# Kernel tuning notes

Hardware: AMD Instinct MI355X
Metric: run time of the kernel (lower is better)

The kernel has to match this reference:

```python
import jax, jax.numpy as jnp
import numpy as np

# ---- static physical configuration (matches init_kwargs param dict) ----
NX = NY = 513
NL = 3
N_ENS = 4
LX = LY = 5120.0e3
DX = LX / (NX - 1)
DY = LY / (NY - 1)
F0 = 9.375e-5
BETA = 1.754e-11
A2 = 0.0
A4 = 2.0e9
DELTA_EK = 2.0
TAU0 = 2.0e-5
BCCO = 0.2
ZFBC = BCCO / (1.0 + 0.5 * BCCO)
DT = 600.0
NUM_STEPS = 4
HEIGHTS = np.array([350.0, 750.0, 2900.0])
RED_G = np.array([0.025, 0.0125])

JAC_COEF = 1.0 / (F0 * DX * DY)
HYPERDIFF_COEF = A4 / F0**2 / DX**6
BOTTOM_FRICTION_COEF = DELTA_EK / (2.0 * abs(F0) * DX**2 * (-HEIGHTS[-1]))


def _build_constants():
    """Precompute stratification / mode / Helmholtz matrices (float64 numpy, cast to f32)."""
    A = np.zeros((NL, NL))
    A[0, 0] = 1.0 / (HEIGHTS[0] * RED_G[0])
    A[0, 1] = -1.0 / (HEIGHTS[0] * RED_G[0])
    for i in range(1, NL - 1):
        A[i, i - 1] = -1.0 / (HEIGHTS[i] * RED_G[i - 1])
        A[i, i] = 1.0 / HEIGHTS[i] * (1.0 / RED_G[i] + 1.0 / RED_G[i - 1])
        A[i, i + 1] = -1.0 / (HEIGHTS[i] * RED_G[i])
    A[-1, -1] = 1.0 / (HEIGHTS[NL - 1] * RED_G[NL - 2])
    A[-1, -2] = -1.0 / (HEIGHTS[NL - 1] * RED_G[NL - 2])
    lam_r, R = np.linalg.eig(A)
    lam_l, L = np.linalg.eig(A.T)
    lam_r, R, lam_l, L = lam_r.real, R.real, lam_l.real, L.real
    # align left eigenvectors with right eigenvalue ordering (biorthogonality)
    order = np.array([int(np.argmin(np.abs(lam_l - lr))) for lr in lam_r])
    L = L[:, order]
    Cl2m = np.diag(1.0 / np.diag(L.T @ R)) @ L.T
    Cm2l = R
    lambd = lam_r
    # DST-I eigenvalues of the 5-point Laplacian on the interior grid
    xg, yg = np.meshgrid(np.arange(1, NX - 1), np.arange(1, NY - 1), indexing='ij')
    lap_dst = (2 * (np.cos(np.pi / (NX - 1) * xg) - 1) / DX**2
               + 2 * (np.cos(np.pi / (NY - 1) * yg) - 1) / DY**2)
    helm_dst = lap_dst[None] / F0**2 - lambd[:, None, None]  # (nl, nx-2, ny-2)

    def np_dstI1D(x):
        N = x.shape[-1]
        xp = np.zeros(x.shape[:-1] + (N + 2,))
        xp[..., 1:-1] = x
        return np.fft.irfft(-1j * xp, n=2 * (N + 1), axis=-1, norm='ortho')[..., 1:N + 1]

    def np_dstI2D(x):
        return np.swapaxes(np_dstI1D(np.swapaxes(np_dstI1D(x), -1, -2)), -1, -2)

    const = np.ones((NL, NX, NY)) / (NX * NY)
    s = np.zeros_like(const)
    s[:, 1:-1, 1:-1] = np_dstI2D(np_dstI2D(const[:, 1:-1, 1:-1]) / helm_dst)
    hom_sol = (const + s * lambd[:, None, None])[:-1]  # (nl-1, nx, ny)
    M = (Cm2l[1:] - Cm2l[:-1])[:NL - 1, :NL - 1] * hom_sol.mean((1, 2))[None, :]
    alpha = -np.linalg.inv(M) @ (Cm2l[1:, :-1] - Cm2l[:-1, :-1])
    # wind forcing: curl(tau)/(f0*H1) on interior points; tau_y = 0, tau_x(y) only
    tau_x = -TAU0 * np.cos(2 * np.pi * (np.arange(NY) + 0.5) / NY)[None, :] * np.ones((NX, NY))
    dtaux_dy = (tau_x[1:-1, 2:] - tau_x[1:-1, :-2]) / (2 * DY)
    wind = (-dtaux_dy / (F0 * HEIGHTS[0]))[None]  # (1, nx-2, ny-2)
    f32 = lambda a: jnp.asarray(a, jnp.float32)
    return dict(A=f32(A), Cl2m=f32(Cl2m), Cm2l=f32(Cm2l), helmoltz_dst=f32(helm_dst),
                alpha_matrix=f32(alpha), homogeneous_sol=f32(hom_sol), wind_forcing=f32(wind))


# ---------------- stencil ops ----------------

def _pad11(x):
    return jnp.pad(x, [(0, 0)] * (x.ndim - 2) + [(1, 1), (1, 1)])


def laplacian_h_nobc(f):
    # unscaled 5-point Laplacian, interior values only: (..., nx-2, ny-2)
    return (f[..., 2:, 1:-1] + f[..., :-2, 1:-1] + f[..., 1:-1, 2:] + f[..., 1:-1, :-2]
            - 4.0 * f[..., 1:-1, 1:-1])


def laplacian_h(f, fc):
    # full-grid Laplacian with partial-slip boundary treatment (coefficient fc = zfbc)
    lap = _pad11(laplacian_h_nobc(f))
    lap = lap.at[..., 0, :].set(fc * (f[..., 1, :] - f[..., 0, :]))
    lap = lap.at[..., -1, :].set(fc * (f[..., -2, :] - f[..., -1, :]))
    lap = lap.at[..., :, 0].set(fc * (f[..., :, 1] - f[..., :, 0]))
    lap = lap.at[..., :, -1].set(fc * (f[..., :, -2] - f[..., :, -1]))
    return lap


def laplacian_h_boundaries(f, fc):
    # boundary Laplacian values, concat order: x=0 (y interior), x=-1, y=0 (full x), y=-1
    return jnp.concatenate([
        fc * (f[..., 1, 1:-1] - f[..., 0, 1:-1]),
        fc * (f[..., -2, 1:-1] - f[..., -1, 1:-1]),
        fc * (f[..., :, 1] - f[..., :, 0]),
        fc * (f[..., :, -2] - f[..., :, -1])], axis=-1)


def jacobi_h(f, g):
    # Arakawa 9-point Jacobian J(f, g), interior values (..., nx-2, ny-2)
    dx_f = f[..., 2:, :] - f[..., :-2, :]
    dx_g = g[..., 2:, :] - g[..., :-2, :]
    dy_f = f[..., 2:] - f[..., :-2]
    dy_g = g[..., 2:] - g[..., :-2]
    return ((dx_f[..., 1:-1] * dy_g[..., 1:-1, :] - dx_g[..., 1:-1] * dy_f[..., 1:-1, :])
            + (f[..., 2:, 1:-1] * dy_g[..., 2:, :] - f[..., :-2, 1:-1] * dy_g[..., :-2, :])
            - (f[..., 1:-1, 2:] * dx_g[..., 2:] - f[..., 1:-1, :-2] * dx_g[..., :-2])
            + (g[..., 1:-1, 2:] * dx_f[..., 2:] - g[..., 1:-1, :-2] * dx_f[..., :-2])
            - (g[..., 2:, 1:-1] * dy_f[..., 2:, :] - g[..., :-2, 1:-1] * dy_f[..., :-2, :])) / 12.0


# ---------------- DST-I elliptic solve ----------------

def dstI1D(x):
    N = x.shape[-1]
    z = jnp.zeros(x.shape[:-1] + (1,), x.dtype)
    xp = jnp.concatenate([z, x, z], axis=-1)
    return jnp.fft.irfft(-1j * xp.astype(jnp.complex64), n=2 * (N + 1), axis=-1,
                         norm='ortho')[..., 1:N + 1]


def dstI2D(x):
    return jnp.swapaxes(dstI1D(jnp.swapaxes(dstI1D(x), -1, -2)), -1, -2)


def inverse_elliptic_dst(f, op_dst):
    return dstI2D(dstI2D(f) / op_dst)


# ---------------- QG time derivative ----------------

def _time_derivatives(y, A, Cl2m, Cm2l, helm_dst, alpha, hom_sol, wind):
    q, p = y[0], y[1]  # (..., nl, nx, ny)
    # advection + hyperdiffusion RHS on interior (a_2 == 0 branch skipped as in source)
    rhs = JAC_COEF * jacobi_h(q, p)
    delta2_p = laplacian_h(p, ZFBC)
    rhs = rhs - HYPERDIFF_COEF * laplacian_h_nobc(laplacian_h(delta2_p, ZFBC))
    rhs = rhs.at[..., 0:1, :, :].add(wind)
    rhs = rhs.at[..., -1:, :, :].add(BOTTOM_FRICTION_COEF * laplacian_h_nobc(p[..., -1:, :, :]))
    dq = _pad11(rhs)
    # layers -> modes, DST Helmholtz inversion, homogeneous-solution correction
    rhs_h = jnp.einsum('ij,...jxy->...ixy', Cl2m, dq)
    dp_modes = _pad11(inverse_elliptic_dst(rhs_h[..., 1:-1, 1:-1], helm_dst))
    mean_m = dp_modes[..., :-1, :, :].mean((-2, -1))  # (..., nl-1)
    dalpha = jnp.einsum('ij,...j->...i', alpha, mean_m)[..., None, None]
    dp_modes = dp_modes.at[..., :-1, :, :].add(dalpha * hom_sol)
    dp = jnp.einsum('ij,...jxy->...ixy', Cm2l, dp_modes)
    # boundary vorticity update
    dp_bound = jnp.concatenate([dp[..., 0, 1:-1], dp[..., -1, 1:-1],
                                dp[..., :, 0], dp[..., :, -1]], axis=-1)
    delta_p_bound = laplacian_h_boundaries(dp / (F0 * DX)**2, ZFBC)
    dq_bound = delta_p_bound - jnp.einsum('ij,...jl->...il', A, dp_bound)
    ny2 = NY - 2
    dq = dq.at[..., 0, 1:-1].set(dq_bound[..., :ny2])
    dq = dq.at[..., -1, 1:-1].set(dq_bound[..., ny2:2 * ny2])
    dq = dq.at[..., :, 0].set(dq_bound[..., 2 * ny2:2 * ny2 + NX])
    dq = dq.at[..., :, -1].set(dq_bound[..., 2 * ny2 + NX:2 * ny2 + 2 * NX])
    return jnp.stack((dq, dp), 0)


def _forecast(y0, t, A, Cl2m, Cm2l, helm_dst, alpha, hom_sol, wind):
    deriv = lambda y: _time_derivatives(y, A, Cl2m, Cm2l, helm_dst, alpha, hom_sol, wind)

    def step(y, dt_):
        k1 = deriv(y)
        k2 = deriv(y + 0.5 * dt_ * k1)
        k3 = deriv(y + 0.5 * dt_ * k2)
        k4 = deriv(y + dt_ * k3)
        y_next = y + (dt_ / 6.0) * (k1 + 2.0 * k2 + 2.0 * k3 + k4)
        return y_next, y_next

    _, traj = jax.lax.scan(step, y0, t[1:] - t[:-1])
    return jnp.concatenate([y0[None], traj], axis=0)  # (T, 2, n_ens, nl, nx, ny)


def setup_inputs() -> dict:
    key = jax.random.key(0)
    y0 = 0.1 * jax.random.normal(key, (2, N_ENS, NL, NX, NY), dtype=jnp.float32)
    t = jnp.arange(NUM_STEPS + 1, dtype=jnp.float32) * DT
    consts = _build_constants()
    return dict(y0=y0, t=t, **consts)


def reference(y0, t, A, Cl2m, Cm2l, helmoltz_dst, alpha_matrix, homogeneous_sol, wind_forcing):
    return _forecast(y0, t, A, Cl2m, Cm2l, helmoltz_dst, alpha_matrix,
                     homogeneous_sol, wind_forcing)
```

## Files before the change

kernel.cpp:

```cpp
#include <hip/hip_runtime.h>
#include <math.h>

#define NXY 513
#define NIN 511
#define NL3 3
#define NE4 4
#define NB 12
#define GLD 512

static constexpr long FS  = (long)NE4 * NL3 * NXY * NXY;
static constexpr long GSZ = (long)NB * GLD * GLD;
static constexpr int  NSTEPS = 4;

static constexpr double dF0 = 9.375e-05;
static constexpr double dDX = 10000.0;
static constexpr float ZFBCf     = (float)(0.2 / (1.0 + 0.5 * 0.2));
static constexpr float JACCf     = (float)(1.0 / (dF0 * dDX * dDX));
static constexpr float HYPCf     = (float)(2.0e9 / (dF0 * dF0) / (dDX*dDX*dDX*dDX*dDX*dDX));
static constexpr float BFCf      = (float)(2.0 / (2.0 * dF0 * dDX * dDX * (-2900.0)));
static constexpr float INVF0DX2f = (float)(1.0 / ((dF0 * dDX) * (dF0 * dDX)));

typedef short  bf16x8 __attribute__((ext_vector_type(8)));
typedef float  f32x4  __attribute__((ext_vector_type(4)));
typedef unsigned int u32;
typedef __attribute__((address_space(1))) const u32 GAS;
typedef __attribute__((address_space(3))) u32 LAS;
#define GLDS(gp, lp) __builtin_amdgcn_global_load_lds((GAS*)(gp), (LAS*)(lp), 16, 0, 0)

__device__ __forceinline__ unsigned short f2bf(float x) {
    unsigned int u = __float_as_uint(x);
    return (unsigned short)((u + 0x7FFFu + ((u >> 16) & 1u)) >> 16);
}
__device__ __forceinline__ float bf2f(unsigned short h) {
    return __uint_as_float(((unsigned int)h) << 16);
}

__global__ void initS_kernel(unsigned short* __restrict__ Sh, unsigned short* __restrict__ Sl) {
    int k = blockIdx.x * 256 + threadIdx.x;
    int n = blockIdx.y;
    if (k >= GLD || n >= GLD) return;
    float v = 0.f;
    if (n < NIN && k < NIN) {
        int m = ((n + 1) * (k + 1)) & 1023;
        v = (float)(0.0625 * sin(M_PI * (double)m / 512.0));
    }
    unsigned short hs = f2bf(v);
    Sh[n * GLD + k] = hs;
    Sl[n * GLD + k] = f2bf(v - bf2f(hs));
}

__global__ __launch_bounds__(256) void fused_rhs(
    float* __restrict__ kq, const float* __restrict__ q, const float* __restrict__ p,
    const float* __restrict__ wind)
{
    __shared__ float ps[22][72];
    __shared__ float qs[22][72];
    __shared__ float l1[22][72];
    __shared__ float l2[22][72];
    const int c  = blockIdx.z;
    const int x0 = 1 + blockIdx.y * 16;
    const int y0 = 1 + blockIdx.x * 64;
    const int t  = threadIdx.x;
    const size_t off = (size_t)c * NXY * NXY;
    const float* pp = p + off;
    const float* qp = q + off;

    for (int idx = t; idx < 22 * 70; idx += 256) {
        int i = idx / 70, j = idx % 70;
        int gx = x0 - 3 + i, gy = y0 - 3 + j;
        bool in = (gx >= 0 && gx < NXY && gy >= 0 && gy < NXY);
        size_t go = (size_t)gx * NXY + gy;
        ps[i][j] = in ? pp[go] : 0.f;
        qs[i][j] = in ? qp[go] : 0.f;
    }
    __syncthreads();

#define LAPBC(a, i, j, gx, gy) \
    ((gy) == 0       ? ZFBCf * (a[i][(j)+1] - a[i][j]) : \
     (gy) == NXY-1   ? ZFBCf * (a[i][(j)-1] - a[i][j]) : \
     (gx) == 0       ? ZFBCf * (a[(i)+1][j] - a[i][j]) : \
     (gx) == NXY-1   ? ZFBCf * (a[(i)-1][j] - a[i][j]) : \
     a[(i)+1][j] + a[(i)-1][j] + a[i][(j)+1] + a[i][(j)-1] - 4.f * a[i][j])

    for (int idx = t; idx < 20 * 68; idx += 256) {
        int i = 1 + idx / 68, j = 1 + idx % 68;
        int gx = x0 - 3 + i, gy = y0 - 3 + j;
        float v = 0.f;
        if (gx >= 0 && gx < NXY && gy >= 0 && gy < NXY) v = LAPBC(ps, i, j, gx, gy);
        l1[i][j] = v;
    }
    __syncthreads();

    for (int idx = t; idx < 18 * 66; idx += 256) {
        int i = 2 + idx / 66, j = 2 + idx % 66;
        int gx = x0 - 3 + i, gy = y0 - 3 + j;
        float v = 0.f;
        if (gx >= 0 && gx < NXY && gy >= 0 && gy < NXY) v = LAPBC(l1, i, j, gx, gy);
        l2[i][j] = v;
    }
    __syncthreads();
#undef LAPBC

    const int l = c % NL3;
    for (int idx = t; idx < 16 * 64; idx += 256) {
        int i = 3 + idx / 64, j = 3 + idx % 64;
        int gx = x0 - 3 + i, gy = y0 - 3 + j;
        if (gx > NIN || gy > NIN) continue;
        float fmm=qs[i-1][j-1], fm0=qs[i-1][j], fmp=qs[i-1][j+1];
        float f0m=qs[i][j-1],                    f0p=qs[i][j+1];
        float fpm=qs[i+1][j-1], fp0=qs[i+1][j], fpp=qs[i+1][j+1];
        float gmm=ps[i-1][j-1], gm0=ps[i-1][j], gmp=ps[i-1][j+1];
        float g0m=ps[i][j-1],   g00=ps[i][j],   g0p=ps[i][j+1];
        float gpm=ps[i+1][j-1], gp0=ps[i+1][j], gpp=ps[i+1][j+1];
        float J1 = (fp0 - fm0) * (g0p - g0m) - (gp0 - gm0) * (f0p - f0m);
        float J2 = fp0 * (gpp - gpm) - fm0 * (gmp - gmm);
        float J3 = f0p * (gpp - gmp) - f0m * (gpm - gmm);
        float J4 = g0p * (fpp - fmp) - g0m * (fpm - fmm);
        float J5 = gp0 * (fpp - fpm) - gm0 * (fmp - fmm);
        float jac = (J1 + J2 - J3 + J4 - J5) * (1.0f / 12.0f);
        float lap3 = l2[i+1][j] + l2[i-1][j] + l2[i][j+1] + l2[i][j-1] - 4.f * l2[i][j];
        float v = JACCf * jac - HYPCf * lap3;
        if (l == 0)       v += wind[(size_t)(gx-1) * NIN + (gy-1)];
        if (l == NL3-1)   v += BFCf * (gp0 + gm0 + g0p + g0m - 4.f * g00);
        kq[off + (size_t)gx * NXY + gy] = v;
    }
}

__global__ void l2m_kernel(unsigned short* __restrict__ Gh, unsigned short* __restrict__ Gl,
                           const float* __restrict__ kq, const float* __restrict__ Cl2m) {
    int ry = blockIdx.x * blockDim.x + threadIdx.x;
    int rx = blockIdx.y * blockDim.y + threadIdx.y;
    int e = blockIdx.z;
    size_t go = (size_t)(e * NL3) * GLD * GLD + (size_t)rx * GLD + ry;
    if (rx >= NIN || ry >= NIN) {
        for (int i = 0; i < 3; ++i) { Gh[go + (size_t)i*GLD*GLD] = 0; Gl[go + (size_t)i*GLD*GLD] = 0; }
        return;
    }
    size_t base = ((size_t)(e * NL3) * NXY + (rx + 1)) * NXY + (ry + 1);
    float f0 = kq[base];
    float f1 = kq[base + (size_t)NXY*NXY];
    float f2 = kq[base + 2*(size_t)NXY*NXY];
    float v[3];
    v[0] = Cl2m[0]*f0 + Cl2m[1]*f1 + Cl2m[2]*f2;
    v[1] = Cl2m[3]*f0 + Cl2m[4]*f1 + Cl2m[5]*f2;
    v[2] = Cl2m[6]*f0 + Cl2m[7]*f1 + Cl2m[8]*f2;
#pragma unroll
    for (int i = 0; i < 3; ++i) {
        unsigned short hs = f2bf(v[i]);
        Gh[go + (size_t)i*GLD*GLD] = hs;
        Gl[go + (size_t)i*GLD*GLD] = f2bf(v[i] - bf2f(hs));
    }
}

#define EPLD 68
__global__ __launch_bounds__(256, 3) void gemm_dst(
    const unsigned short* __restrict__ Ah, const unsigned short* __restrict__ Al,
    const unsigned short* __restrict__ Sh, const unsigned short* __restrict__ Sl,
    unsigned short* __restrict__ Ch, unsigned short* __restrict__ Cl,
    float* __restrict__ Cf, const float* __restrict__ helm)
{
    __shared__ __attribute__((aligned(16))) char ldsraw[32768];
    float* ep = (float*)ldsraw;
    const int id = blockIdx.x;
    const int nblk = id / 96, rr = id - nblk * 96;
    const int b = rr >> 3, mblk = rr & 7;
    const int m0 = mblk << 6, n0 = nblk << 6;
    const int t = threadIdx.x;
    const int wave = t >> 6, lane = t & 63;
    const int wr = wave >> 1, wc = wave & 1;
    const int lr = lane & 15, g = lane >> 4;
    const unsigned short* Abh = Ah + (size_t)b * 262144;
    const unsigned short* Abl = Al + (size_t)b * 262144;

    const int srow = t >> 2;
    const int scol = ((t & 3) ^ ((srow >> 1) & 3)) * 8;
    const size_t gAe = (size_t)(m0 + srow) * 512 + scol;
    const size_t gBe = (size_t)(n0 + srow) * 512 + scol;
    const int ldbase = wave * 1024;

    auto STAGE = [&](int buf, int kt) {
        char* bb = ldsraw + buf * 16384;
        int ke = kt * 32;
        GLDS(Abh + gAe + ke, bb + ldbase);
        GLDS(Abl + gAe + ke, bb + 4096 + ldbase);
        GLDS(Sh  + gBe + ke, bb + 8192 + ldbase);
        GLDS(Sl  + gBe + ke, bb + 12288 + ldbase);
    };

    f32x4 acc[2][2] = {};
    int abyte[2], bbyte[2];
#pragma unroll
    for (int i = 0; i < 2; ++i) {
        int ar = wr*32 + i*16 + lr;
        abyte[i] = ar*64 + ((g ^ ((ar >> 1) & 3)) * 16);
    }
#pragma unroll
    for (int j = 0; j < 2; ++j) {
        int br = wc*32 + j*16 + lr;
        bbyte[j] = 8192 + br*64 + ((g ^ ((br >> 1) & 3)) * 16);
    }

    STAGE(0, 0);
    __syncthreads();
    for (int it = 0; it < 16; ++it) {
        const int buf = it & 1;
        if (it < 15) STAGE(buf ^ 1, it + 1);
        const char* bb = ldsraw + buf * 16384;
        bf16x8 fbh[2], fbl[2];
#pragma unroll
        for (int j = 0; j < 2; ++j) {
            fbh[j] = *(const bf16x8*)(bb + bbyte[j]);
            fbl[j] = *(const bf16x8*)(bb + 4096 + bbyte[j]);
        }
#pragma unroll
        for (int i = 0; i < 2; ++i) {
            bf16x8 fah = *(const bf16x8*)(bb + abyte[i]);
            bf16x8 fal = *(const bf16x8*)(bb + 4096 + abyte[i]);
#pragma unroll
            for (int j = 0; j < 2; ++j) {
                acc[i][j] = __builtin_amdgcn_mfma_f32_16x16x32_bf16(fah, fbh[j], acc[i][j], 0, 0, 0);
                acc[i][j] = __builtin_amdgcn_mfma_f32_16x16x32_bf16(fah, fbl[j], acc[i][j], 0, 0, 0);
                acc[i][j] = __builtin_amdgcn_mfma_f32_16x16x32_bf16(fal, fbh[j], acc[i][j], 0, 0, 0);
            }
        }
        __syncthreads();
    }

    const int mode = b % NL3;
    const float* hp = helm ? (helm + (size_t)mode * NIN * NIN) : nullptr;
#pragma unroll
    for (int i = 0; i < 2; ++i) {
        int mml = wr*32 + i*16 + 4*g;
#pragma unroll
        for (int j = 0; j < 2; ++j) {
            int nnl = wc*32 + j*16 + lr;
            int nn = n0 + nnl;
            float v[4];
#pragma unroll
            for (int r = 0; r < 4; ++r) v[r] = acc[i][j][r];
            if (hp && nn < NIN) {
                int mmb = m0 + mml;
#pragma unroll
                for (int r = 0; r < 4; ++r)
                    if (mmb + r < NIN) v[r] /= hp[(size_t)nn*NIN + mmb + r];
            }
#pragma unroll
            for (int r = 0; r < 4; ++r) ep[nnl*EPLD + mml + r] = v[r];
        }
    }
    __syncthreads();

#pragma unroll
    for (int c = 0; c < 2; ++c) {
        int chunk = t + 256*c;
        int row = chunk >> 3;
        int cb  = (chunk & 7) * 8;
        float v[8];
#pragma unroll
        for (int k = 0; k < 8; ++k) v[k] = ep[row*EPLD + cb + k];
        size_t co = (size_t)b*262144 + (size_t)(n0 + row)*512 + m0 + cb;
        if (Cf) {
            f32x4 v0 = {v[0], v[1], v[2], v[3]};
            f32x4 v1 = {v[4], v[5], v[6], v[7]};
            *(f32x4*)(Cf + co)     = v0;
            *(f32x4*)(Cf + co + 4) = v1;
        } else {
            unsigned int h[4], lo[4];
#pragma unroll
            for (int k = 0; k < 4; ++k) {
                unsigned short h0 = f2bf(v[2*k]), h1 = f2bf(v[2*k+1]);
                unsigned short l0 = f2bf(v[2*k]-bf2f(h0)), l1 = f2bf(v[2*k+1]-bf2f(h1));
                h[k]  = (unsigned int)h0 | ((unsigned int)h1 << 16);
                lo[k] = (unsigned int)l0 | ((unsigned int)l1 << 16);
            }
            *(uint4*)(Ch + co) = make_uint4(h[0], h[1], h[2], h[3]);
            *(uint4*)(Cl + co) = make_uint4(lo[0], lo[1], lo[2], lo[3]);
        }
    }
}

__global__ void mean_kernel(float* __restrict__ partial, const float* __restrict__ G) {
    int gy = blockIdx.y;
    int e = gy >> 1, m = gy & 1;
    const float* g = G + (size_t)(e * NL3 + m) * GLD * GLD;
    float s = 0.f;
    for (int idx = blockIdx.x * 256 + threadIdx.x; idx < GLD*GLD; idx += 64 * 256)
        s += g[idx];
    __shared__ float red[256];
    red[threadIdx.x] = s; __syncthreads();
    for (int w = 128; w >= 1; w >>= 1) {
        if (threadIdx.x < w) red[threadIdx.x] += red[threadIdx.x + w];
        __syncthreads();
    }
    if (threadIdx.x == 0) partial[gy * 64 + blockIdx.x] = red[0];
}

__global__ void dalpha_kernel(float* __restrict__ dal, const float* __restrict__ partial,
                              const float* __restrict__ alpha) {
    int t = threadIdx.x;
    if (t >= 8) return;
    int e = t >> 1, i = t & 1;
    float s0 = 0.f, s1 = 0.f;
    for (int bk = 0; bk < 64; ++bk) { s0 += partial[(e*2+0)*64 + bk]; s1 += partial[(e*2+1)*64 + bk]; }
    const float inv = 1.0f / ((float)NXY * (float)NXY);
    dal[t] = alpha[i*2+0] * (s0 * inv) + alpha[i*2+1] * (s1 * inv);
}

__global__ void m2l_kernel(float* __restrict__ kp, const float* __restrict__ G,
                           const float* __restrict__ dal, const float* __restrict__ hom,
                           const float* __restrict__ Cm2l) {
    int y = blockIdx.x * blockDim.x + threadIdx.x;
    int x = blockIdx.y * blockDim.y + threadIdx.y;
    int e = blockIdx.z;
    if (x >= NXY || y >= NXY) return;
    float mv[3];
    bool interior = (x >= 1 && x <= NIN && y >= 1 && y <= NIN);
#pragma unroll
    for (int i = 0; i < 3; ++i)
        mv[i] = interior ? G[(size_t)(e*NL3 + i) * GLD * GLD + (size_t)(x-1) * GLD + (y-1)] : 0.f;
    float h0 = hom[(size_t)x * NXY + y];
    float h1 = hom[(size_t)NXY*NXY + (size_t)x * NXY + y];
    mv[0] += dal[e*2 + 0] * h0;
    mv[1] += dal[e*2 + 1] * h1;
#pragma unroll
    for (int l = 0; l < 3; ++l)
        kp[((size_t)(e*NL3 + l) * NXY + x) * NXY + y] =
            Cm2l[l*3+0]*mv[0] + Cm2l[l*3+1]*mv[1] + Cm2l[l*3+2]*mv[2];
}

__global__ void bound_kernel(float* __restrict__ kq, const float* __restrict__ kp,
                             const float* __restrict__ Amat) {
    int pos = blockIdx.x * 256 + threadIdx.x;
    int e = blockIdx.y;
    if (pos >= 2048) return;
    int x, y, xn, yn;
    if (pos < NIN)            { x = 0;      y = pos + 1;        xn = 1;      yn = y; }
    else if (pos < 2*NIN)     { x = NXY-1;  y = pos - NIN + 1;  xn = NXY-2;  yn = y; }
    else if (pos < 2*NIN+NXY) { x = pos - 2*NIN;       y = 0;      xn = x; yn = 1; }
    else                      { x = pos - (2*NIN+NXY); y = NXY-1;  xn = x; yn = NXY-2; }
    float dpb[3], lpb[3];
#pragma unroll
    for (int j = 0; j < 3; ++j) {
        const float* f = kp + (size_t)(e*NL3 + j) * NXY * NXY;
        float c = f[(size_t)x * NXY + y];
        float nb = f[(size_t)xn * NXY + yn];
        dpb[j] = c;
        lpb[j] = ZFBCf * INVF0DX2f * (nb - c);
    }
#pragma unroll
    for (int l = 0; l < 3; ++l) {
        float v = lpb[l] - (Amat[l*3+0]*dpb[0] + Amat[l*3+1]*dpb[1] + Amat[l*3+2]*dpb[2]);
        kq[((size_t)(e*NL3 + l) * NXY + x) * NXY + y] = v;
    }
}

__global__ void rk_fused(float4* __restrict__ o1, float4* __restrict__ o2,
                         const float4* __restrict__ x, const float4* __restrict__ k,
                         float c1, float c2, int accumulate,
                         const float* __restrict__ t, int s, long n4) {
    float dt = t[s+1] - t[s];
    float a1 = c1 * dt, a2 = c2 * dt;
    for (long i = (long)blockIdx.x * blockDim.x + threadIdx.x; i < n4;
         i += (long)gridDim.x * blockDim.x) {
        float4 kk = k[i], xx = x[i];
        float4 b0 = accumulate ? o1[i] : xx;
        o1[i] = make_float4(b0.x + a1*kk.x, b0.y + a1*kk.y, b0.z + a1*kk.z, b0.w + a1*kk.w);
        if (o2) o2[i] = make_float4(xx.x + a2*kk.x, xx.y + a2*kk.y, xx.z + a2*kk.z, xx.w + a2*kk.w);
    }
}

__global__ void copy_kernel(float4* __restrict__ out, const float4* __restrict__ in, long n4) {
    for (long i = (long)blockIdx.x * blockDim.x + threadIdx.x; i < n4;
         i += (long)gridDim.x * blockDim.x)
        out[i] = in[i];
}

extern "C" void kernel_launch(void* const* d_in, const int* in_sizes, int n_in,
                              void* d_out, int out_size, void* d_ws, size_t ws_size,
                              hipStream_t stream) {
    const float* y0    = (const float*)d_in[0];
    const float* tarr  = (const float*)d_in[1];
    const float* Amat  = (const float*)d_in[2];
    const float* Cl2m  = (const float*)d_in[3];
    const float* Cm2l  = (const float*)d_in[4];
    const float* helm  = (const float*)d_in[5];
    const float* alpha = (const float*)d_in[6];
    const float* hom   = (const float*)d_in[7];
    const float* wind  = (const float*)d_in[8];
    float* out = (float*)d_out;
    char* base = (char*)d_ws;

    unsigned short* Sh = (unsigned short*)base;
    unsigned short* Sl = (unsigned short*)(base + 512*1024);
    float* ytmp = (float*)(base + 1024*1024);
    float* kbuf = ytmp + 2*FS;
    char*  REGb = (char*)(kbuf + 2*FS);
    unsigned short* P0h = (unsigned short*)REGb;
    unsigned short* P0l = P0h + GSZ;
    unsigned short* P1h = P0l + GSZ;
    unsigned short* P1l = P1h + GSZ;
    float* R4 = (float*)REGb;
    float* partial = (float*)(REGb + (size_t)2*FS*sizeof(float));
    float* dal = partial + 512;

    const dim3 bSt(64, 4, 1);
    const dim3 gSt4((NXY + 63)/64, (NXY + 3)/4, NE4);
    const dim3 gL2M(8, 128, NE4);
    const dim3 gF(8, 32, NB);
    const dim3 gG(768, 1, 1);
    const long n4 = 2*FS/4;

    initS_kernel<<<dim3(2, GLD), 256, 0, stream>>>(Sh, Sl);
    copy_kernel<<<1024, 256, 0, stream>>>((float4*)out, (const float4*)y0, n4);

    auto deriv = [&](const float* y, float* k) {
        const float* q = y;  const float* p = y + FS;
        float* kq = k;       float* kp = k + FS;
        fused_rhs<<<gF, 256, 0, stream>>>(kq, q, p, wind);
        l2m_kernel<<<gL2M, bSt, 0, stream>>>(P0h, P0l, kq, Cl2m);
        gemm_dst<<<gG, 256, 0, stream>>>(P0h, P0l, Sh, Sl, P1h, P1l, nullptr, nullptr);
        gemm_dst<<<gG, 256, 0, stream>>>(P1h, P1l, Sh, Sl, P0h, P0l, nullptr, helm);
        gemm_dst<<<gG, 256, 0, stream>>>(P0h, P0l, Sh, Sl, P1h, P1l, nullptr, nullptr);
        gemm_dst<<<gG, 256, 0, stream>>>(P1h, P1l, Sh, Sl, nullptr, nullptr, R4, nullptr);
        mean_kernel<<<dim3(64, 8), 256, 0, stream>>>(partial, R4);
        dalpha_kernel<<<1, 64, 0, stream>>>(dal, partial, alpha);
        m2l_kernel<<<gSt4, bSt, 0, stream>>>(kp, R4, dal, hom, Cm2l);
        bound_kernel<<<dim3(8, NE4), 256, 0, stream>>>(kq, kp, Amat);
    };

    for (int s = 0; s < NSTEPS; ++s) {
        float* ycur  = out + (size_t)s * 2 * FS;
        float* ynext = out + (size_t)(s + 1) * 2 * FS;
        deriv(ycur, kbuf);
        rk_fused<<<1024, 256, 0, stream>>>((float4*)ynext, (float4*)ytmp, (const float4*)ycur,
                                           (const float4*)kbuf, 1.f/6.f, 0.5f, 0, tarr, s, n4);
        deriv(ytmp, kbuf);
        rk_fused<<<1024, 256, 0, stream>>>((float4*)ynext, (float4*)ytmp, (const float4*)ycur,
                                           (const float4*)kbuf, 2.f/6.f, 0.5f, 1, tarr, s, n4);
        deriv(ytmp, kbuf);
        rk_fused<<<1024, 256, 0, stream>>>((float4*)ynext, (float4*)ytmp, (const float4*)ycur,
                                           (const float4*)kbuf, 2.f/6.f, 1.0f, 1, tarr, s, n4);
        deriv(ytmp, kbuf);
        rk_fused<<<1024, 256, 0, stream>>>((float4*)ynext, nullptr, (const float4*)ycur,
                                           (const float4*)kbuf, 1.f/6.f, 0.f, 1, tarr, s, n4);
    }
}
```

Baseline: 2.264 ms.

## Fuse RHS with layer-to-mode projection, and mean and RK update into epilogues

The Jacobian/hyperdiffusion RHS kernel now loops over all three layers per tile and projects to modes directly into the bf16 GEMM input, which removes the separate l2m pass. The last DST GEMM computes per-block partial sums in its epilogue, replacing the mean and dalpha kernels. A single mega kernel now does mode-to-layer conversion, the boundary condition and the RK stage update together, so the full k buffer is never materialised and the standalone RK kernel goes away. This cuts launches and global-memory round trips. In exchange the RHS kernel has fewer blocks and more serial work per block, and boundary points recompute a neighbour's mode values.

Result: slower. 2.352 ms (+3.9%).

```diff
diff --git a/kernel.cpp b/kernel.cpp
--- a/kernel.cpp
+++ b/kernel.cpp
@@ -49,31 +49,21 @@
     Sl[n * GLD + k] = f2bf(v - bf2f(hs));
 }
 
-__global__ __launch_bounds__(256) void fused_rhs(
-    float* __restrict__ kq, const float* __restrict__ q, const float* __restrict__ p,
-    const float* __restrict__ wind)
+__global__ __launch_bounds__(256) void fused_rhs_l2m(
+    float* __restrict__ kq, unsigned short* __restrict__ Gh, unsigned short* __restrict__ Gl,
+    const float* __restrict__ y, const float* __restrict__ wind, const float* __restrict__ Cl2m)
 {
     __shared__ float ps[22][72];
     __shared__ float qs[22][72];
     __shared__ float l1[22][72];
     __shared__ float l2[22][72];
-    const int c  = blockIdx.z;
+    const int e  = blockIdx.z;
     const int x0 = 1 + blockIdx.y * 16;
     const int y0 = 1 + blockIdx.x * 64;
     const int t  = threadIdx.x;
-    const size_t off = (size_t)c * NXY * NXY;
-    const float* pp = p + off;
-    const float* qp = q + off;
-
-    for (int idx = t; idx < 22 * 70; idx += 256) {
-        int i = idx / 70, j = idx % 70;
-        int gx = x0 - 3 + i, gy = y0 - 3 + j;
-        bool in = (gx >= 0 && gx < NXY && gy >= 0 && gy < NXY);
-        size_t go = (size_t)gx * NXY + gy;
-        ps[i][j] = in ? pp[go] : 0.f;
-        qs[i][j] = in ? qp[go] : 0.f;
-    }
-    __syncthreads();
+    const float* q = y;
+    const float* p = y + FS;
+    float rhs[4][3];
 
 #define LAPBC(a, i, j, gx, gy) \
     ((gy) == 0       ? ZFBCf * (a[i][(j)+1] - a[i][j]) : \
@@ -82,73 +72,90 @@
      (gx) == NXY-1   ? ZFBCf * (a[(i)-1][j] - a[i][j]) : \
      a[(i)+1][j] + a[(i)-1][j] + a[i][(j)+1] + a[i][(j)-1] - 4.f * a[i][j])
 
-    for (int idx = t; idx < 20 * 68; idx += 256) {
-        int i = 1 + idx / 68, j = 1 + idx % 68;
-        int gx = x0 - 3 + i, gy = y0 - 3 + j;
-        float v = 0.f;
-        if (gx >= 0 && gx < NXY && gy >= 0 && gy < NXY) v = LAPBC(ps, i, j, gx, gy);
-        l1[i][j] = v;
-    }
-    __syncthreads();
-
-    for (int idx = t; idx < 18 * 66; idx += 256) {
-        int i = 2 + idx / 66, j = 2 + idx % 66;
-        int gx = x0 - 3 + i, gy = y0 - 3 + j;
-        float v = 0.f;
-        if (gx >= 0 && gx < NXY && gy >= 0 && gy < NXY) v = LAPBC(l1, i, j, gx, gy);
-        l2[i][j] = v;
-    }
-    __syncthreads();
+#pragma unroll
+    for (int l = 0; l < 3; ++l) {
+        __syncthreads();
+        const int c = e * NL3 + l;
+        const size_t off = (size_t)c * NXY * NXY;
+        const float* pp = p + off;
+        const float* qp = q + off;
+        for (int idx = t; idx < 22 * 70; idx += 256) {
+            int i = idx / 70, j = idx % 70;
+            int gx = x0 - 3 + i, gy = y0 - 3 + j;
+            bool in = (gx >= 0 && gx < NXY && gy >= 0 && gy < NXY);
+            size_t go = (size_t)gx * NXY + gy;
+            ps[i][j] = in ? pp[go] : 0.f;
+            qs[i][j] = in ? qp[go] : 0.f;
+        }
+        __syncthreads();
+        for (int idx = t; idx < 20 * 68; idx += 256) {
+            int i = 1 + idx / 68, j = 1 + idx % 68;
+            int gx = x0 - 3 + i, gy = y0 - 3 + j;
+            float v = 0.f;
+            if (gx >= 0 && gx < NXY && gy >= 0 && gy < NXY) v = LAPBC(ps, i, j, gx, gy);
+            l1[i][j] = v;
+        }
+        __syncthreads();
+        for (int idx = t; idx < 18 * 66; idx += 256) {
+            int i = 2 + idx / 66, j = 2 + idx % 66;
+            int gx = x0 - 3 + i, gy = y0 - 3 + j;
+            float v = 0.f;
+            if (gx >= 0 && gx < NXY && gy >= 0 && gy < NXY) v = LAPBC(l1, i, j, gx, gy);
+            l2[i][j] = v;
+        }
+        __syncthreads();
+#pragma unroll
+        for (int u = 0; u < 4; ++u) {
+            int idx = t + 256 * u;
+            int i = 3 + idx / 64, j = 3 + idx % 64;
+            int gx = x0 - 3 + i, gy = y0 - 3 + j;
+            if (gx > NIN || gy > NIN) { rhs[u][l] = 0.f; continue; }
+            float fmm=qs[i-1][j-1], fm0=qs[i-1][j], fmp=qs[i-1][j+1];
+            float f0m=qs[i][j-1],                    f0p=qs[i][j+1];
+            float fpm=qs[i+1][j-1], fp0=qs[i+1][j], fpp=qs[i+1][j+1];
+            float gmm=ps[i-1][j-1], gm0=ps[i-1][j], gmp=ps[i-1][j+1];
+            float g0m=ps[i][j-1],   g00=ps[i][j],   g0p=ps[i][j+1];
+            float gpm=ps[i+1][j-1], gp0=ps[i+1][j], gpp=ps[i+1][j+1];
+            float J1 = (fp0 - fm0) * (g0p - g0m) - (gp0 - gm0) * (f0p - f0m);
+            float J2 = fp0 * (gpp - gpm) - fm0 * (gmp - gmm);
+            float J3 = f0p * (gpp - gmp) - f0m * (gpm - gmm);
+            float J4 = g0p * (fpp - fmp) - g0m * (fpm - fmm);
+            float J5 = gp0 * (fpp - fpm) - gm0 * (fmp - fmm);
+            float jac = (J1 + J2 - J3 + J4 - J5) * (1.0f / 12.0f);
+            float lap3 = l2[i+1][j] + l2[i-1][j] + l2[i][j+1] + l2[i][j-1] - 4.f * l2[i][j];
+            float v = JACCf * jac - HYPCf * lap3;
+            if (l == 0)       v += wind[(size_t)(gx-1) * NIN + (gy-1)];
+            if (l == NL3-1)   v += BFCf * (gp0 + gm0 + g0p + g0m - 4.f * g00);
+            rhs[u][l] = v;
+            kq[off + (size_t)gx * NXY + gy] = v;
+        }
+    }
 #undef LAPBC
 
-    const int l = c % NL3;
-    for (int idx = t; idx < 16 * 64; idx += 256) {
+#pragma unroll
+    for (int u = 0; u < 4; ++u) {
+        int idx = t + 256 * u;
         int i = 3 + idx / 64, j = 3 + idx % 64;
         int gx = x0 - 3 + i, gy = y0 - 3 + j;
-        if (gx > NIN || gy > NIN) continue;
-        float fmm=qs[i-1][j-1], fm0=qs[i-1][j], fmp=qs[i-1][j+1];
-        float f0m=qs[i][j-1],                    f0p=qs[i][j+1];
-        float fpm=qs[i+1][j-1], fp0=qs[i+1][j], fpp=qs[i+1][j+1];
-        float gmm=ps[i-1][j-1], gm0=ps[i-1][j], gmp=ps[i-1][j+1];
-        float g0m=ps[i][j-1],   g00=ps[i][j],   g0p=ps[i][j+1];
-        float gpm=ps[i+1][j-1], gp0=ps[i+1][j], gpp=ps[i+1][j+1];
-        float J1 = (fp0 - fm0) * (g0p - g0m) - (gp0 - gm0) * (f0p - f0m);
-        float J2 = fp0 * (gpp - gpm) - fm0 * (gmp - gmm);
-        float J3 = f0p * (gpp - gmp) - f0m * (gpm - gmm);
-        float J4 = g0p * (fpp - fmp) - g0m * (fpm - fmm);
-        float J5 = gp0 * (fpp - fpm) - gm0 * (fmp - fmm);
-        float jac = (J1 + J2 - J3 + J4 - J5) * (1.0f / 12.0f);
-        float lap3 = l2[i+1][j] + l2[i-1][j] + l2[i][j+1] + l2[i][j-1] - 4.f * l2[i][j];
-        float v = JACCf * jac - HYPCf * lap3;
-        if (l == 0)       v += wind[(size_t)(gx-1) * NIN + (gy-1)];
-        if (l == NL3-1)   v += BFCf * (gp0 + gm0 + g0p + g0m - 4.f * g00);
-        kq[off + (size_t)gx * NXY + gy] = v;
-    }
-}
-
-__global__ void l2m_kernel(unsigned short* __restrict__ Gh, unsigned short* __restrict__ Gl,
-                           const float* __restrict__ kq, const float* __restrict__ Cl2m) {
-    int ry = blockIdx.x * blockDim.x + threadIdx.x;
-    int rx = blockIdx.y * blockDim.y + threadIdx.y;
-    int e = blockIdx.z;
-    size_t go = (size_t)(e * NL3) * GLD * GLD + (size_t)rx * GLD + ry;
-    if (rx >= NIN || ry >= NIN) {
-        for (int i = 0; i < 3; ++i) { Gh[go + (size_t)i*GLD*GLD] = 0; Gl[go + (size_t)i*GLD*GLD] = 0; }
-        return;
-    }
-    size_t base = ((size_t)(e * NL3) * NXY + (rx + 1)) * NXY + (ry + 1);
-    float f0 = kq[base];
-    float f1 = kq[base + (size_t)NXY*NXY];
-    float f2 = kq[base + 2*(size_t)NXY*NXY];
-    float v[3];
-    v[0] = Cl2m[0]*f0 + Cl2m[1]*f1 + Cl2m[2]*f2;
-    v[1] = Cl2m[3]*f0 + Cl2m[4]*f1 + Cl2m[5]*f2;
-    v[2] = Cl2m[6]*f0 + Cl2m[7]*f1 + Cl2m[8]*f2;
-#pragma unroll
-    for (int i = 0; i < 3; ++i) {
-        unsigned short hs = f2bf(v[i]);
-        Gh[go + (size_t)i*GLD*GLD] = hs;
-        Gl[go + (size_t)i*GLD*GLD] = f2bf(v[i] - bf2f(hs));
+        size_t go = (size_t)(e * NL3) * GLD * GLD + (size_t)(gx-1) * GLD + (gy-1);
+        if (gx > NIN || gy > NIN) {
+#pragma unroll
+            for (int m = 0; m < 3; ++m) {
+                Gh[go + (size_t)m*GLD*GLD] = 0; Gl[go + (size_t)m*GLD*GLD] = 0;
+            }
+            continue;
+        }
+        float f0 = rhs[u][0], f1 = rhs[u][1], f2 = rhs[u][2];
+        float v[3];
+        v[0] = Cl2m[0]*f0 + Cl2m[1]*f1 + Cl2m[2]*f2;
+        v[1] = Cl2m[3]*f0 + Cl2m[4]*f1 + Cl2m[5]*f2;
+        v[2] = Cl2m[6]*f0 + Cl2m[7]*f1 + Cl2m[8]*f2;
+#pragma unroll
+        for (int m = 0; m < 3; ++m) {
+            unsigned short hs = f2bf(v[m]);
+            Gh[go + (size_t)m*GLD*GLD] = hs;
+            Gl[go + (size_t)m*GLD*GLD] = f2bf(v[m] - bf2f(hs));
+        }
     }
 }
 
@@ -157,9 +164,10 @@
     const unsigned short* __restrict__ Ah, const unsigned short* __restrict__ Al,
     const unsigned short* __restrict__ Sh, const unsigned short* __restrict__ Sl,
     unsigned short* __restrict__ Ch, unsigned short* __restrict__ Cl,
-    float* __restrict__ Cf, const float* __restrict__ helm)
+    float* __restrict__ Cf, const float* __restrict__ helm, float* __restrict__ part)
 {
     __shared__ __attribute__((aligned(16))) char ldsraw[32768];
+    __shared__ float red[256];
     float* ep = (float*)ldsraw;
     const int id = blockIdx.x;
     const int nblk = id / 96, rr = id - nblk * 96;
@@ -250,6 +258,7 @@
     }
     __syncthreads();
 
+    float lsum = 0.f;
 #pragma unroll
     for (int c = 0; c < 2; ++c) {
         int chunk = t + 256*c;
@@ -260,6 +269,8 @@
         for (int k = 0; k < 8; ++k) v[k] = ep[row*EPLD + cb + k];
         size_t co = (size_t)b*262144 + (size_t)(n0 + row)*512 + m0 + cb;
         if (Cf) {
+#pragma unroll
+            for (int k = 0; k < 8; ++k) lsum += v[k];
             f32x4 v0 = {v[0], v[1], v[2], v[3]};
             f32x4 v1 = {v[4], v[5], v[6], v[7]};
             *(f32x4*)(Cf + co)     = v0;
@@ -277,95 +288,104 @@
             *(uint4*)(Cl + co) = make_uint4(lo[0], lo[1], lo[2], lo[3]);
         }
     }
-}
-
-__global__ void mean_kernel(float* __restrict__ partial, const float* __restrict__ G) {
-    int gy = blockIdx.y;
-    int e = gy >> 1, m = gy & 1;
-    const float* g = G + (size_t)(e * NL3 + m) * GLD * GLD;
-    float s = 0.f;
-    for (int idx = blockIdx.x * 256 + threadIdx.x; idx < GLD*GLD; idx += 64 * 256)
-        s += g[idx];
-    __shared__ float red[256];
-    red[threadIdx.x] = s; __syncthreads();
-    for (int w = 128; w >= 1; w >>= 1) {
-        if (threadIdx.x < w) red[threadIdx.x] += red[threadIdx.x + w];
-        __syncthreads();
-    }
-    if (threadIdx.x == 0) partial[gy * 64 + blockIdx.x] = red[0];
-}
-
-__global__ void dalpha_kernel(float* __restrict__ dal, const float* __restrict__ partial,
-                              const float* __restrict__ alpha) {
-    int t = threadIdx.x;
-    if (t >= 8) return;
-    int e = t >> 1, i = t & 1;
-    float s0 = 0.f, s1 = 0.f;
-    for (int bk = 0; bk < 64; ++bk) { s0 += partial[(e*2+0)*64 + bk]; s1 += partial[(e*2+1)*64 + bk]; }
-    const float inv = 1.0f / ((float)NXY * (float)NXY);
-    dal[t] = alpha[i*2+0] * (s0 * inv) + alpha[i*2+1] * (s1 * inv);
-}
-
-__global__ void m2l_kernel(float* __restrict__ kp, const float* __restrict__ G,
-                           const float* __restrict__ dal, const float* __restrict__ hom,
-                           const float* __restrict__ Cm2l) {
-    int y = blockIdx.x * blockDim.x + threadIdx.x;
-    int x = blockIdx.y * blockDim.y + threadIdx.y;
-    int e = blockIdx.z;
-    if (x >= NXY || y >= NXY) return;
-    float mv[3];
-    bool interior = (x >= 1 && x <= NIN && y >= 1 && y <= NIN);
-#pragma unroll
-    for (int i = 0; i < 3; ++i)
-        mv[i] = interior ? G[(size_t)(e*NL3 + i) * GLD * GLD + (size_t)(x-1) * GLD + (y-1)] : 0.f;
-    float h0 = hom[(size_t)x * NXY + y];
-    float h1 = hom[(size_t)NXY*NXY + (size_t)x * NXY + y];
-    mv[0] += dal[e*2 + 0] * h0;
-    mv[1] += dal[e*2 + 1] * h1;
-#pragma unroll
-    for (int l = 0; l < 3; ++l)
-        kp[((size_t)(e*NL3 + l) * NXY + x) * NXY + y] =
-            Cm2l[l*3+0]*mv[0] + Cm2l[l*3+1]*mv[1] + Cm2l[l*3+2]*mv[2];
-}
-
-__global__ void bound_kernel(float* __restrict__ kq, const float* __restrict__ kp,
-                             const float* __restrict__ Amat) {
-    int pos = blockIdx.x * 256 + threadIdx.x;
-    int e = blockIdx.y;
-    if (pos >= 2048) return;
-    int x, y, xn, yn;
-    if (pos < NIN)            { x = 0;      y = pos + 1;        xn = 1;      yn = y; }
-    else if (pos < 2*NIN)     { x = NXY-1;  y = pos - NIN + 1;  xn = NXY-2;  yn = y; }
-    else if (pos < 2*NIN+NXY) { x = pos - 2*NIN;       y = 0;      xn = x; yn = 1; }
-    else                      { x = pos - (2*NIN+NXY); y = NXY-1;  xn = x; yn = NXY-2; }
-    float dpb[3], lpb[3];
-#pragma unroll
-    for (int j = 0; j < 3; ++j) {
-        const float* f = kp + (size_t)(e*NL3 + j) * NXY * NXY;
-        float c = f[(size_t)x * NXY + y];
-        float nb = f[(size_t)xn * NXY + yn];
-        dpb[j] = c;
-        lpb[j] = ZFBCf * INVF0DX2f * (nb - c);
-    }
+
+    if (part && mode < 2) {
+        red[t] = lsum;
+        __syncthreads();
+        for (int w = 128; w >= 1; w >>= 1) {
+            if (t < w) red[t] += red[t + w];
+            __syncthreads();
+        }
+        if (t == 0) {
+            int plane8 = (b / NL3) * 2 + mode;
+            part[plane8 * 64 + nblk * 8 + mblk] = red[0];
+        }
+    }
+}
+
+__global__ __launch_bounds__(256) void m2l_mega(
+    float* __restrict__ ynext, float* __restrict__ ytmp,
+    const float* __restrict__ ycur, const float* __restrict__ kq,
+    const float* __restrict__ G, const float* __restrict__ hom,
+    const float* __restrict__ Cm2l, const float* __restrict__ Amat,
+    const float* __restrict__ alpha, const float* __restrict__ part,
+    const float* __restrict__ tarr, int s, float c1, float c2, int accumulate)
+{
+    __shared__ float sp[128];
+    __shared__ float sdal[2];
+    const int yy = blockIdx.x * 64 + threadIdx.x;
+    const int xx = blockIdx.y * 4 + threadIdx.y;
+    const int e  = blockIdx.z;
+    const int tt = threadIdx.y * 64 + threadIdx.x;
+    const bool act = (xx < NXY && yy < NXY);
+
+    if (tt < 128) sp[tt] = part[(e*2 + (tt >> 6))*64 + (tt & 63)];
+    __syncthreads();
+    if (tt == 0) {
+        float s0 = 0.f, s1 = 0.f;
+        for (int j = 0; j < 64; ++j) { s0 += sp[j]; s1 += sp[64 + j]; }
+        const float inv = 1.0f / ((float)NXY * (float)NXY);
+        float mm0 = s0 * inv, mm1 = s1 * inv;
+        sdal[0] = alpha[0]*mm0 + alpha[1]*mm1;
+        sdal[1] = alpha[2]*mm0 + alpha[3]*mm1;
+    }
+    __syncthreads();
+    if (!act) return;
+    const float dal0 = sdal[0], dal1 = sdal[1];
+
+    auto DP = [&](int px, int py, float* dp) {
+        bool inter = (px >= 1 && px <= NIN && py >= 1 && py <= NIN);
+        float mv0 = 0.f, mv1 = 0.f, mv2 = 0.f;
+        if (inter) {
+            size_t gb = (size_t)(e*NL3)*GLD*GLD + (size_t)(px-1)*GLD + (py-1);
+            mv0 = G[gb]; mv1 = G[gb + (size_t)GLD*GLD]; mv2 = G[gb + 2*(size_t)GLD*GLD];
+        }
+        mv0 += dal0 * hom[(size_t)px*NXY + py];
+        mv1 += dal1 * hom[(size_t)NXY*NXY + (size_t)px*NXY + py];
+        dp[0] = Cm2l[0]*mv0 + Cm2l[1]*mv1 + Cm2l[2]*mv2;
+        dp[1] = Cm2l[3]*mv0 + Cm2l[4]*mv1 + Cm2l[5]*mv2;
+        dp[2] = Cm2l[6]*mv0 + Cm2l[7]*mv1 + Cm2l[8]*mv2;
+    };
+
+    float dp[3];
+    DP(xx, yy, dp);
+
+    const bool bnd = (xx == 0 || xx == NXY-1 || yy == 0 || yy == NXY-1);
+    float kqv[3];
+    if (!bnd) {
+#pragma unroll
+        for (int l = 0; l < 3; ++l)
+            kqv[l] = kq[((size_t)(e*NL3 + l)*NXY + xx)*NXY + yy];
+    } else {
+        int xn, yn;
+        if      (yy == 0)      { xn = xx;    yn = 1; }
+        else if (yy == NXY-1)  { xn = xx;    yn = NXY-2; }
+        else if (xx == 0)      { xn = 1;     yn = yy; }
+        else                   { xn = NXY-2; yn = yy; }
+        float dpn[3];
+        DP(xn, yn, dpn);
+#pragma unroll
+        for (int l = 0; l < 3; ++l) {
+            float lpb = ZFBCf * INVF0DX2f * (dpn[l] - dp[l]);
+            kqv[l] = lpb - (Amat[l*3+0]*dp[0] + Amat[l*3+1]*dp[1] + Amat[l*3+2]*dp[2]);
+        }
+    }
+
+    const float dt = tarr[s+1] - tarr[s];
+    const float a1 = c1 * dt, a2 = c2 * dt;
 #pragma unroll
     for (int l = 0; l < 3; ++l) {
-        float v = lpb[l] - (Amat[l*3+0]*dpb[0] + Amat[l*3+1]*dpb[1] + Amat[l*3+2]*dpb[2]);
-        kq[((size_t)(e*NL3 + l) * NXY + x) * NXY + y] = v;
-    }
-}
-
-__global__ void rk_fused(float4* __restrict__ o1, float4* __restrict__ o2,
-                         const float4* __restrict__ x, const float4* __restrict__ k,
-                         float c1, float c2, int accumulate,
-                         const float* __restrict__ t, int s, long n4) {
-    float dt = t[s+1] - t[s];
-    float a1 = c1 * dt, a2 = c2 * dt;
-    for (long i = (long)blockIdx.x * blockDim.x + threadIdx.x; i < n4;
-         i += (long)gridDim.x * blockDim.x) {
-        float4 kk = k[i], xx = x[i];
-        float4 b0 = accumulate ? o1[i] : xx;
-        o1[i] = make_float4(b0.x + a1*kk.x, b0.y + a1*kk.y, b0.z + a1*kk.z, b0.w + a1*kk.w);
-        if (o2) o2[i] = make_float4(xx.x + a2*kk.x, xx.y + a2*kk.y, xx.z + a2*kk.z, xx.w + a2*kk.w);
+        size_t oq = ((size_t)(e*NL3 + l)*NXY + xx)*NXY + yy;
+        size_t op = oq + FS;
+        float xq = ycur[oq], xp = ycur[op];
+        float bq = accumulate ? ynext[oq] : xq;
+        float bp = accumulate ? ynext[op] : xp;
+        ynext[oq] = bq + a1 * kqv[l];
+        ynext[op] = bp + a1 * dp[l];
+        if (ytmp) {
+            ytmp[oq] = xq + a2 * kqv[l];
+            ytmp[op] = xp + a2 * dp[l];
+        }
     }
 }
 
@@ -393,55 +413,41 @@
     unsigned short* Sh = (unsigned short*)base;
     unsigned short* Sl = (unsigned short*)(base + 512*1024);
     float* ytmp = (float*)(base + 1024*1024);
-    float* kbuf = ytmp + 2*FS;
-    char*  REGb = (char*)(kbuf + 2*FS);
+    float* kq   = ytmp + 2*FS;
+    char*  REGb = (char*)(kq + FS);
     unsigned short* P0h = (unsigned short*)REGb;
     unsigned short* P0l = P0h + GSZ;
     unsigned short* P1h = P0l + GSZ;
     unsigned short* P1l = P1h + GSZ;
     float* R4 = (float*)REGb;
     float* partial = (float*)(REGb + (size_t)2*FS*sizeof(float));
-    float* dal = partial + 512;
 
     const dim3 bSt(64, 4, 1);
-    const dim3 gSt4((NXY + 63)/64, (NXY + 3)/4, NE4);
-    const dim3 gL2M(8, 128, NE4);
-    const dim3 gF(8, 32, NB);
+    const dim3 gM(9, 129, NE4);
+    const dim3 gF(8, 32, NE4);
     const dim3 gG(768, 1, 1);
     const long n4 = 2*FS/4;
 
     initS_kernel<<<dim3(2, GLD), 256, 0, stream>>>(Sh, Sl);
     copy_kernel<<<1024, 256, 0, stream>>>((float4*)out, (const float4*)y0, n4);
 
-    auto deriv = [&](const float* y, float* k) {
-        const float* q = y;  const float* p = y + FS;
-        float* kq = k;       float* kp = k + FS;
-        fused_rhs<<<gF, 256, 0, stream>>>(kq, q, p, wind);
-        l2m_kernel<<<gL2M, bSt, 0, stream>>>(P0h, P0l, kq, Cl2m);
-        gemm_dst<<<gG, 256, 0, stream>>>(P0h, P0l, Sh, Sl, P1h, P1l, nullptr, nullptr);
-        gemm_dst<<<gG, 256, 0, stream>>>(P1h, P1l, Sh, Sl, P0h, P0l, nullptr, helm);
-        gemm_dst<<<gG, 256, 0, stream>>>(P0h, P0l, Sh, Sl, P1h, P1l, nullptr, nullptr);
-        gemm_dst<<<gG, 256, 0, stream>>>(P1h, P1l, Sh, Sl, nullptr, nullptr, R4, nullptr);
-        mean_kernel<<<dim3(64, 8), 256, 0, stream>>>(partial, R4);
-        dalpha_kernel<<<1, 64, 0, stream>>>(dal, partial, alpha);
-        m2l_kernel<<<gSt4, bSt, 0, stream>>>(kp, R4, dal, hom, Cm2l);
-        bound_kernel<<<dim3(8, NE4), 256, 0, stream>>>(kq, kp, Amat);
+    auto evalstep = [&](const float* y, const float* ycur, float* ynext, float* otmp,
+                        int s, float c1, float c2, int accumulate) {
+        fused_rhs_l2m<<<gF, 256, 0, stream>>>(kq, P0h, P0l, y, wind, Cl2m);
+        gemm_dst<<<gG, 256, 0, stream>>>(P0h, P0l, Sh, Sl, P1h, P1l, nullptr, nullptr, nullptr);
+        gemm_dst<<<gG, 256, 0, stream>>>(P1h, P1l, Sh, Sl, P0h, P0l, nullptr, helm, nullptr);
+        gemm_dst<<<gG, 256, 0, stream>>>(P0h, P0l, Sh, Sl, P1h, P1l, nullptr, nullptr, nullptr);
+        gemm_dst<<<gG, 256, 0, stream>>>(P1h, P1l, Sh, Sl, nullptr, nullptr, R4, nullptr, partial);
+        m2l_mega<<<gM, bSt, 0, stream>>>(ynext, otmp, ycur, kq, R4, hom, Cm2l, Amat,
+                                         alpha, partial, tarr, s, c1, c2, accumulate);
     };
 
     for (int s = 0; s < NSTEPS; ++s) {
         float* ycur  = out + (size_t)s * 2 * FS;
         float* ynext = out + (size_t)(s + 1) * 2 * FS;
-        deriv(ycur, kbuf);
-        rk_fused<<<1024, 256, 0, stream>>>((float4*)ynext, (float4*)ytmp, (const float4*)ycur,
-                                           (const float4*)kbuf, 1.f/6.f, 0.5f, 0, tarr, s, n4);
-        deriv(ytmp, kbuf);
-        rk_fused<<<1024, 256, 0, stream>>>((float4*)ynext, (float4*)ytmp, (const float4*)ycur,
-                                           (const float4*)kbuf, 2.f/6.f, 0.5f, 1, tarr, s, n4);
-        deriv(ytmp, kbuf);
-        rk_fused<<<1024, 256, 0, stream>>>((float4*)ynext, (float4*)ytmp, (const float4*)ycur,
-                                           (const float4*)kbuf, 2.f/6.f, 1.0f, 1, tarr, s, n4);
-        deriv(ytmp, kbuf);
-        rk_fused<<<1024, 256, 0, stream>>>((float4*)ynext, nullptr, (const float4*)ycur,
-                                           (const float4*)kbuf, 1.f/6.f, 0.f, 1, tarr, s, n4);
-    }
-}
+        evalstep(ycur, ycur, ynext, ytmp, s, 1.f/6.f, 0.5f, 0);
+        evalstep(ytmp, ycur, ynext, ytmp, s, 2.f/6.f, 0.5f, 1);
+        evalstep(ytmp, ycur, ynext, ytmp, s, 2.f/6.f, 1.0f, 1);
+        evalstep(ytmp, ycur, ynext, nullptr, s, 1.f/6.f, 0.f, 1);
+    }
+}
```
